# Kernel optimization log

Hardware: AMD Instinct MI355X
Metric: run time of the kernel (lower is better)

Reference implementation:

```python
import jax, jax.numpy as jnp
import numpy as np

NC = 1_000_000   # children
NP_ = 100_000    # parents
DIM = 64         # value/channel dim
H = 4            # heads
DQK = 8          # per-head query/key dim
DH = DQK * H     # 32
RPE = 9          # edge_attr feature dim
SCALE = DQK ** -0.5


def setup_inputs() -> dict:
    key = jax.random.key(0)
    ks = jax.random.split(key, 12)
    return {
        "x_child": jax.random.normal(ks[0], (NC, DIM), dtype=jnp.float32),
        "x_parent": jax.random.normal(ks[1], (NP_, DIM), dtype=jnp.float32),
        "index": jax.random.randint(ks[2], (NC,), 0, NP_, dtype=jnp.int64),
        "edge_attr": jax.random.normal(ks[3], (NC, RPE), dtype=jnp.float32),
        "wq": jax.random.normal(ks[4], (DIM, DH), dtype=jnp.float32) * 0.05,
        "bq": jax.random.normal(ks[5], (DH,), dtype=jnp.float32) * 0.05,
        "wkv": jax.random.normal(ks[6], (DIM, DH + DIM), dtype=jnp.float32) * 0.05,
        "bkv": jax.random.normal(ks[7], (DH + DIM,), dtype=jnp.float32) * 0.05,
        "wk_rpe": jax.random.normal(ks[8], (RPE, DH), dtype=jnp.float32) * 0.05,
        "bk_rpe": jax.random.normal(ks[9], (DH,), dtype=jnp.float32) * 0.05,
        "wq_rpe": jax.random.normal(ks[10], (RPE, DH), dtype=jnp.float32) * 0.05,
        "bq_rpe": jax.random.normal(ks[11], (DH,), dtype=jnp.float32) * 0.05,
    }


def reference(x_child, x_parent, index, edge_attr,
              wq, bq, wkv, bkv, wk_rpe, bk_rpe, wq_rpe, bq_rpe):
    Nc = x_child.shape[0]
    Np = x_parent.shape[0]
    # _get_query: Linear(Cp -> H*DQK) on parents, then gather per child edge
    q_parent = x_parent @ wq + bq                      # (Np, H*D)
    q = q_parent[index].reshape(Nc, H, DQK) * SCALE    # (Nc, H, D)
    # kv projection on children
    kv = x_child @ wkv + bkv                           # (Nc, H*D + DIM)
    k = kv[:, :DH].reshape(Nc, H, DQK)
    v = kv[:, DH:].reshape(Nc, H, DIM // H)
    # relative positional encodings added to k and q
    k = k + (edge_attr @ wk_rpe + bk_rpe).reshape(Nc, H, DQK)
    q = q + (edge_attr @ wq_rpe + bq_rpe).reshape(Nc, H, DQK)
    # per-edge compatibility, segment softmax grouped by parent index
    compat = jnp.einsum('nhd,nhd->nh', q, k)           # (Nc, H)
    m = jax.ops.segment_max(compat, index, num_segments=Np)   # (Np, H)
    e = jnp.exp(compat - m[index])
    s = jax.ops.segment_sum(e, index, num_segments=Np)        # (Np, H)
    attn = e / (s[index] + 1e-16)                      # (Nc, H)
    # weighted scatter-sum pooling
    xw = (v * attn[:, :, None]).reshape(Nc, DIM)       # (Nc, DIM)
    out = jax.ops.segment_sum(xw, index, num_segments=Np)     # (Np, DIM)
    return out
```

## Files before the change

kernel.cpp:

```cpp
#include <hip/hip_runtime.h>

#define NC    1000000
#define NPAR  100000
#define DIM   64
#define H     4
#define RPE   9
#define SCALE 0.35355339059327373f
#define CB    128
#define NBS   ((NPAR + 1023) / 1024)

typedef __attribute__((ext_vector_type(8))) short short8;
typedef __attribute__((ext_vector_type(4))) float f32x4;

__device__ inline unsigned short f2bf(float f) {
    unsigned int u = __float_as_uint(f);
    u += 0x7fff + ((u >> 16) & 1);
    return (unsigned short)(u >> 16);
}
__device__ inline unsigned int pack2bf(float a, float b) {
    return (unsigned int)f2bf(a) | ((unsigned int)f2bf(b) << 16);
}

__global__ __launch_bounds__(256) void qproj_kernel(const float* __restrict__ xp,
                             const float* __restrict__ wq,
                             const float* __restrict__ bq,
                             float* __restrict__ qp) {
    __shared__ float wqT[32 * 64];
    __shared__ float bqL[32];
    int tid = threadIdx.x;
    for (int i = tid; i < 2048; i += 256) { int o = i >> 6, j = i & 63; wqT[i] = wq[j * 32 + o]; }
    if (tid < 32) bqL[tid] = bq[tid];
    __syncthreads();
    int p = blockIdx.x * 256 + tid;
    if (p >= NPAR) return;
    float4 x4[16];
    const float4* xr = (const float4*)(xp + (size_t)p * 64);
#pragma unroll
    for (int i = 0; i < 16; ++i) x4[i] = xr[i];
    float* qpr = qp + (size_t)p * 32;
#pragma unroll 1
    for (int o = 0; o < 32; ++o) {
        float acc = bqL[o];
        const float4* w4 = (const float4*)(wqT + o * 64);
#pragma unroll
        for (int j = 0; j < 16; ++j) { float4 w = w4[j], xx = x4[j];
            acc += xx.x * w.x + xx.y * w.y + xx.z * w.z + xx.w * w.w; }
        qpr[o] = acc * SCALE;
    }
}

__global__ __launch_bounds__(256) void prepB_kernel(
    const float* __restrict__ wkv, const float* __restrict__ bkv,
    const float* __restrict__ wkr, const float* __restrict__ bkr,
    const float* __restrict__ wqr, const float* __restrict__ bqr,
    uint4* __restrict__ Bg) {
    int tid = threadIdx.x;
    for (int i = tid; i < 12 * 128; i += 256) {
        int kb = i >> 7, n = i & 127;
        float w[8];
#pragma unroll
        for (int jj = 0; jj < 8; ++jj) {
            int k = kb * 8 + jj;
            float val = 0.f;
            if (n < 32) {
                if (k < 64)       val = wkv[k * 96 + n];
                else if (k < 73)  val = wkr[(k - 64) * 32 + n];
                else if (k == 73) val = bkv[n] + bkr[n];
            } else if (n < 96) {
                int d = n - 32;
                if (k < 64)       val = wkv[k * 96 + 32 + d];
                else if (k == 73) val = bkv[32 + d];
            } else {
                int o = n - 96;
                if (k >= 64 && k < 73) val = wqr[(k - 64) * 32 + o];
                else if (k == 73)      val = bqr[o];
            }
            w[jj] = val;
        }
        uint4 v;
        v.x = pack2bf(w[0], w[1]); v.y = pack2bf(w[2], w[3]);
        v.z = pack2bf(w[4], w[5]); v.w = pack2bf(w[6], w[7]);
        Bg[kb * 128 + n] = v;
    }
}

__global__ __launch_bounds__(256) void hist_kernel(const int* __restrict__ index,
                            int* __restrict__ cnt) {
    int c = blockIdx.x * 256 + threadIdx.x;
    if (c >= NC) return;
    atomicAdd(&cnt[index[c]], 1);
}

__global__ __launch_bounds__(1024) void scanA_kernel(const int* __restrict__ cnt,
                                                     int* __restrict__ bsum) {
    __shared__ int red[16];
    int i = blockIdx.x * 1024 + threadIdx.x;
    int v = (i < NPAR) ? cnt[i] : 0;
#pragma unroll
    for (int off = 32; off; off >>= 1) v += __shfl_down(v, off, 64);
    if ((threadIdx.x & 63) == 0) red[threadIdx.x >> 6] = v;
    __syncthreads();
    if (threadIdx.x < 16) {
        int s = red[threadIdx.x];
#pragma unroll
        for (int off = 8; off; off >>= 1) s += __shfl_down(s, off, 16);
        if (threadIdx.x == 0) bsum[blockIdx.x] = s;
    }
}

__global__ __launch_bounds__(128) void scanB_kernel(int* __restrict__ bsum) {
    __shared__ int s[128];
    int t = threadIdx.x;
    int v = (t < NBS) ? bsum[t] : 0;
    s[t] = v;
    __syncthreads();
    for (int off = 1; off < 128; off <<= 1) {
        int x = s[t];
        int add = (t >= off) ? s[t - off] : 0;
        __syncthreads();
        s[t] = x + add;
        __syncthreads();
    }
    if (t < NBS) bsum[t] = s[t] - v;
}

__global__ __launch_bounds__(1024) void scanC_kernel(const int* __restrict__ cnt,
                                                     const int* __restrict__ bsum,
                                                     int* __restrict__ rowStart,
                                                     int* __restrict__ cursor) {
    __shared__ int s[1024];
    int t = threadIdx.x;
    int i = blockIdx.x * 1024 + t;
    int v = (i < NPAR) ? cnt[i] : 0;
    s[t] = v;
    __syncthreads();
    for (int off = 1; off < 1024; off <<= 1) {
        int x = s[t];
        int add = (t >= off) ? s[t - off] : 0;
        __syncthreads();
        s[t] = x + add;
        __syncthreads();
    }
    int excl = s[t] - v + bsum[blockIdx.x];
    if (i < NPAR) { rowStart[i] = excl; cursor[i] = excl; }
    if (i == NPAR - 1) rowStart[NPAR] = excl + v;
}

__global__ __launch_bounds__(256) void scatter_kernel(const int* __restrict__ index,
                               int* __restrict__ cursor,
                               int* __restrict__ order) {
    int c = blockIdx.x * 256 + threadIdx.x;
    if (c >= NC) return;
    order[atomicAdd(&cursor[index[c]], 1)] = c;
}

__global__ __launch_bounds__(256, 4) void fused_kernel(
    const float* __restrict__ xc, const float* __restrict__ ea_g,
    const int* __restrict__ index, const int* __restrict__ order,
    const int* __restrict__ rowStart,
    const uint4* __restrict__ Bg,
    const float* __restrict__ qp,
    float* __restrict__ outw, float* __restrict__ sW)
{
    __shared__ __align__(16) char R1[34816];
    __shared__ float e_lds[CB * 4];
    __shared__ int par_s[CB];
    __shared__ int wcnt[4];
    __shared__ int segStart[130];

    uint4* A4 = (uint4*)R1;
    float* kqT = (float*)R1;
    float* wvS = (float*)R1;

    const int tid  = threadIdx.x;
    const int lane = tid & 63, wave = tid >> 6;
    const int col  = lane & 15, quad = lane >> 4;
    const int G    = blockIdx.x * CB;
    const int validCB = min(NC - G, CB);

    {
        const int half = tid >> 7;
        const int c = tid & 127;
        const bool valid = c < validCB;
        int ch = 0, p = 0x7fffffff;
        if (valid) { ch = order[G + c]; p = index[ch]; }
        if (half == 0) {
            par_s[c] = p;
            float4 x4[10];
            if (valid) {
                const float4* xr = (const float4*)(xc + (size_t)ch * 64);
#pragma unroll
                for (int i = 0; i < 10; ++i) x4[i] = xr[i];
            } else {
#pragma unroll
                for (int i = 0; i < 10; ++i) x4[i] = make_float4(0.f, 0.f, 0.f, 0.f);
            }
#pragma unroll
            for (int kb = 0; kb < 5; ++kb) {
                uint4 v;
                v.x = pack2bf(x4[kb * 2].x, x4[kb * 2].y);
                v.y = pack2bf(x4[kb * 2].z, x4[kb * 2].w);
                v.z = pack2bf(x4[kb * 2 + 1].x, x4[kb * 2 + 1].y);
                v.w = pack2bf(x4[kb * 2 + 1].z, x4[kb * 2 + 1].w);
                A4[kb * 128 + c] = v;
            }
        } else {
            float4 x4[6];
            float ear[9];
            if (valid) {
                const float4* xr = (const float4*)(xc + (size_t)ch * 64);
#pragma unroll
                for (int i = 0; i < 6; ++i) x4[i] = xr[10 + i];
                const float* er = ea_g + (size_t)ch * 9;
#pragma unroll
                for (int r = 0; r < 9; ++r) ear[r] = er[r];
            } else {
#pragma unroll
                for (int i = 0; i < 6; ++i) x4[i] = make_float4(0.f, 0.f, 0.f, 0.f);
#pragma unroll
                for (int r = 0; r < 9; ++r) ear[r] = 0.f;
            }
#pragma unroll
            for (int kb = 0; kb < 3; ++kb) {
                uint4 v;
                v.x = pack2bf(x4[kb * 2].x, x4[kb * 2].y);
                v.y = pack2bf(x4[kb * 2].z, x4[kb * 2].w);
                v.z = pack2bf(x4[kb * 2 + 1].x, x4[kb * 2 + 1].y);
                v.w = pack2bf(x4[kb * 2 + 1].z, x4[kb * 2 + 1].w);
                A4[(5 + kb) * 128 + c] = v;
            }
            {
                uint4 v;
                v.x = pack2bf(ear[0], ear[1]); v.y = pack2bf(ear[2], ear[3]);
                v.z = pack2bf(ear[4], ear[5]); v.w = pack2bf(ear[6], ear[7]);
                A4[8 * 128 + c] = v;
            }
            {
                uint4 v;
                v.x = pack2bf(ear[8], valid ? 1.f : 0.f);
                v.y = 0u; v.z = 0u; v.w = 0u;
                A4[9 * 128 + c] = v;
            }
        }
    }
    __syncthreads();

    f32x4 acc[2][8];
#pragma unroll
    for (int mt = 0; mt < 2; ++mt)
#pragma unroll
        for (int nt = 0; nt < 8; ++nt) acc[mt][nt] = (f32x4){0.f, 0.f, 0.f, 0.f};
    const int wbase = wave * 32;
    const short8* As = (const short8*)A4;
    const short8* Bs = (const short8*)Bg;
    const short8 zero8 = {0, 0, 0, 0, 0, 0, 0, 0};
#pragma unroll 1
    for (int ks = 0; ks < 3; ++ks) {
        const int kb = ks * 4 + quad;
        short8 af0 = zero8, af1 = zero8;
        if (kb < 10) {
            af0 = As[kb * 128 + wbase + col];
            af1 = As[kb * 128 + wbase + 16 + col];
        }
        short8 bf[8];
#pragma unroll
        for (int nt = 0; nt < 6; ++nt) bf[nt] = Bs[kb * 128 + nt * 16 + col];
#pragma unroll
        for (int nt = 0; nt < 6; ++nt) {
            acc[0][nt] = __builtin_amdgcn_mfma_f32_16x16x32_bf16(af0, bf[nt], acc[0][nt], 0, 0, 0);
            acc[1][nt] = __builtin_amdgcn_mfma_f32_16x16x32_bf16(af1, bf[nt], acc[1][nt], 0, 0, 0);
        }
        if (ks == 2) {
#pragma unroll
            for (int nt = 6; nt < 8; ++nt) {
                short8 b2 = Bs[kb * 128 + nt * 16 + col];
                acc[0][nt] = __builtin_amdgcn_mfma_f32_16x16x32_bf16(af0, b2, acc[0][nt], 0, 0, 0);
                acc[1][nt] = __builtin_amdgcn_mfma_f32_16x16x32_bf16(af1, b2, acc[1][nt], 0, 0, 0);
            }
        }
    }
    __syncthreads();

#pragma unroll
    for (int mt = 0; mt < 2; ++mt) {
        int cb = wbase + mt * 16 + quad * 4;
#pragma unroll
        for (int nt = 0; nt < 2; ++nt) {
            int nl = nt * 16 + col;
            *(f32x4*)(kqT + nl * 132 + cb) = acc[mt][nt];
        }
#pragma unroll
        for (int nt = 6; nt < 8; ++nt) {
            int nl = 32 + (nt - 6) * 16 + col;
            *(f32x4*)(kqT + nl * 132 + cb) = acc[mt][nt];
        }
    }
    __syncthreads();

    {
        const int c = tid;
        bool valid = c < validCB;
        int p = 0x7fffffff;
        if (valid) p = par_s[c];
        float e0 = 0.f, e1 = 0.f, e2 = 0.f, e3 = 0.f;
        if (valid) {
            const float* qpr = qp + (size_t)p * 32;
            float qv[32];
#pragma unroll
            for (int i = 0; i < 8; ++i) *(float4*)(qv + 4 * i) = ((const float4*)qpr)[i];
            float comp[4] = {0.f, 0.f, 0.f, 0.f};
#pragma unroll
            for (int o = 0; o < 32; ++o) {
                float kk = kqT[o * 132 + c];
                float qq = qv[o] + kqT[(32 + o) * 132 + c];
                comp[o >> 3] += qq * kk;
            }
            e0 = __expf(comp[0]); e1 = __expf(comp[1]);
            e2 = __expf(comp[2]); e3 = __expf(comp[3]);
        }
        if (c < CB) *(float4*)(e_lds + c * 4) = make_float4(e0, e1, e2, e3);

        bool ishead = valid && (c == 0 || par_s[c - 1] != p);
        unsigned long long mask = __ballot(ishead);
        if (lane == 0) wcnt[wave] = __popcll(mask);
        __syncthreads();
        int base = 0;
#pragma unroll
        for (int w = 0; w < 4; ++w) if (w < wave) base += wcnt[w];
        if (ishead) segStart[base + __popcll(mask & ((1ull << lane) - 1))] = c;
        if (tid == 0) {
            int ns = wcnt[0] + wcnt[1] + wcnt[2] + wcnt[3];
            segStart[ns] = validCB;
            segStart[129] = ns;
        }
    }

#pragma unroll
    for (int mt = 0; mt < 2; ++mt) {
        int cb = wbase + mt * 16 + quad * 4;
#pragma unroll
        for (int nt = 2; nt < 6; ++nt) {
            int d = (nt - 2) * 16 + col;
            int h = nt - 2;
#pragma unroll
            for (int r = 0; r < 4; ++r) {
                float e = e_lds[(cb + r) * 4 + h];
                wvS[(cb + r) * 68 + d] = acc[mt][nt][r] * e;
            }
        }
    }
    __syncthreads();

    {
        int nseg = segStart[129];
        for (int s = wave; s < nseg; s += 4) {
            int a = segStart[s], b = segStart[s + 1];
            int p = par_s[a];
            int d = lane, h = lane >> 4;
            float vs = 0.f, es = 0.f;
            for (int c2 = a; c2 < b; ++c2) {
                vs += wvS[c2 * 68 + d];
                es += e_lds[c2 * 4 + h];
            }
            bool full = (rowStart[p] == G + a) && (rowStart[p + 1] == G + b);
            if (full) {
                outw[(size_t)p * 64 + d] = vs;
                if ((d & 15) == 0) sW[(size_t)p * 4 + h] = es;
            } else {
                atomicAdd(&outw[(size_t)p * 64 + d], vs);
                if ((d & 15) == 0) atomicAdd(&sW[(size_t)p * 4 + h], es);
            }
        }
    }
}

__global__ __launch_bounds__(256) void norm_kernel(const float* __restrict__ sW,
                                                   float* __restrict__ out) {
    int t = blockIdx.x * 256 + threadIdx.x;
    if (t >= NPAR * 64) return;
    out[t] = out[t] / (sW[(t >> 6) * 4 + ((t >> 4) & 3)] + 1e-16f);
}

extern "C" void kernel_launch(void* const* d_in, const int* in_sizes, int n_in,
                              void* d_out, int out_size, void* d_ws, size_t ws_size,
                              hipStream_t stream) {
    const float* xc   = (const float*)d_in[0];
    const float* xp   = (const float*)d_in[1];
    const int*   idx  = (const int*)d_in[2];
    const float* ea   = (const float*)d_in[3];
    const float* wq   = (const float*)d_in[4];
    const float* bq   = (const float*)d_in[5];
    const float* wkv  = (const float*)d_in[6];
    const float* bkv  = (const float*)d_in[7];
    const float* wkr  = (const float*)d_in[8];
    const float* bkr  = (const float*)d_in[9];
    const float* wqr  = (const float*)d_in[10];
    const float* bqr  = (const float*)d_in[11];
    float* out = (float*)d_out;

    char* base = (char*)d_ws;
    size_t off = 0;
    auto alloc = [&](size_t bytes) {
        void* r = base + off;
        off += (bytes + 255) & ~(size_t)255;
        return r;
    };
    float* qp       = (float*)alloc((size_t)NPAR * 32 * sizeof(float));
    int*   cnt      = (int*)  alloc((size_t)NPAR * sizeof(int));
    int*   rowStart = (int*)  alloc(((size_t)NPAR + 1) * sizeof(int));
    int*   cursor   = (int*)  alloc((size_t)NPAR * sizeof(int));
    int*   order    = (int*)  alloc((size_t)NC * sizeof(int));
    float* sW       = (float*)alloc((size_t)NPAR * 4 * sizeof(float));
    int*   bsum     = (int*)  alloc((size_t)NBS * sizeof(int));
    uint4* Bg       = (uint4*)alloc((size_t)12 * 128 * sizeof(uint4));
    (void)ws_size;

    hipMemsetAsync(cnt, 0, (size_t)NPAR * sizeof(int), stream);
    hipMemsetAsync(sW,  0, (size_t)NPAR * 4 * sizeof(float), stream);
    hipMemsetAsync(out, 0, (size_t)NPAR * 64 * sizeof(float), stream);

    qproj_kernel  <<<(NPAR + 255) / 256, 256, 0, stream>>>(xp, wq, bq, qp);
    prepB_kernel  <<<1,                  256, 0, stream>>>(wkv, bkv, wkr, bkr, wqr, bqr, Bg);
    hist_kernel   <<<(NC + 255) / 256,   256, 0, stream>>>(idx, cnt);
    scanA_kernel  <<<NBS,               1024, 0, stream>>>(cnt, bsum);
    scanB_kernel  <<<1,                  128, 0, stream>>>(bsum);
    scanC_kernel  <<<NBS,               1024, 0, stream>>>(cnt, bsum, rowStart, cursor);
    scatter_kernel<<<(NC + 255) / 256,   256, 0, stream>>>(idx, cursor, order);
    fused_kernel  <<<(NC + CB - 1) / CB, 256, 0, stream>>>(xc, ea, idx, order, rowStart,
                                                           Bg, qp, out, sW);
    norm_kernel   <<<(NPAR * 64 + 255) / 256, 256, 0, stream>>>(sW, out);
}
```

Baseline: 660.1 us.

## Store child and parent together in sort order and compute scores from MFMA registers

The scatter kernel now writes (child, parent) pairs, so the fused kernel no longer does a dependent random gather of index[child] after reading the order array. The q·k compatibility is now computed straight from the MFMA accumulator registers, using per-lane q loads and cross-lane shuffle reductions. This removes the LDS transpose store, a barrier, and the column-wise LDS reads. The cost is twice the bytes for the order array and more scattered small global loads of qp per lane.

```diff
diff --git a/kernel.cpp b/kernel.cpp
--- a/kernel.cpp
+++ b/kernel.cpp
@@ -148,15 +148,17 @@
 
 __global__ __launch_bounds__(256) void scatter_kernel(const int* __restrict__ index,
                                int* __restrict__ cursor,
-                               int* __restrict__ order) {
+                               int2* __restrict__ ordCP) {
     int c = blockIdx.x * 256 + threadIdx.x;
     if (c >= NC) return;
-    order[atomicAdd(&cursor[index[c]], 1)] = c;
+    int p = index[c];
+    int pos = atomicAdd(&cursor[p], 1);
+    ordCP[pos] = make_int2(c, p);
 }
 
 __global__ __launch_bounds__(256, 4) void fused_kernel(
     const float* __restrict__ xc, const float* __restrict__ ea_g,
-    const int* __restrict__ index, const int* __restrict__ order,
+    const int2* __restrict__ ordCP,
     const int* __restrict__ rowStart,
     const uint4* __restrict__ Bg,
     const float* __restrict__ qp,
@@ -169,7 +171,6 @@
     __shared__ int segStart[130];
 
     uint4* A4 = (uint4*)R1;
-    float* kqT = (float*)R1;
     float* wvS = (float*)R1;
 
     const int tid  = threadIdx.x;
@@ -183,7 +184,7 @@
         const int c = tid & 127;
         const bool valid = c < validCB;
         int ch = 0, p = 0x7fffffff;
-        if (valid) { ch = order[G + c]; p = index[ch]; }
+        if (valid) { int2 cp = ordCP[G + c]; ch = cp.x; p = cp.y; }
         if (half == 0) {
             par_s[c] = p;
             float4 x4[10];
@@ -281,46 +282,45 @@
     }
     __syncthreads();
 
-#pragma unroll
-    for (int mt = 0; mt < 2; ++mt) {
-        int cb = wbase + mt * 16 + quad * 4;
-#pragma unroll
-        for (int nt = 0; nt < 2; ++nt) {
-            int nl = nt * 16 + col;
-            *(f32x4*)(kqT + nl * 132 + cb) = acc[mt][nt];
-        }
-#pragma unroll
-        for (int nt = 6; nt < 8; ++nt) {
-            int nl = 32 + (nt - 6) * 16 + col;
-            *(f32x4*)(kqT + nl * 132 + cb) = acc[mt][nt];
-        }
-    }
-    __syncthreads();
-
     {
+        float comp[2][4][2];
+#pragma unroll
+        for (int mt = 0; mt < 2; ++mt) {
+#pragma unroll
+            for (int r = 0; r < 4; ++r) {
+                int cc = wbase + mt * 16 + quad * 4 + r;
+                int p = par_s[cc];
+                if (p >= NPAR) p = 0;
+                const float* qpr = qp + (size_t)p * 32;
+#pragma unroll
+                for (int nt = 0; nt < 2; ++nt) {
+                    float q = qpr[nt * 16 + col] + acc[mt][nt + 6][r];
+                    comp[mt][r][nt] = acc[mt][nt][r] * q;
+                }
+            }
+        }
+#pragma unroll
+        for (int m = 1; m < 8; m <<= 1) {
+#pragma unroll
+            for (int mt = 0; mt < 2; ++mt)
+#pragma unroll
+                for (int r = 0; r < 4; ++r)
+#pragma unroll
+                    for (int nt = 0; nt < 2; ++nt)
+                        comp[mt][r][nt] += __shfl_xor(comp[mt][r][nt], m, 64);
+        }
+        {
+            int idx = col & 7;
+            int mtS = idx >> 2, rS = idx & 3;
+            int cS = wbase + mtS * 16 + quad * 4 + rS;
+            int hb = col >> 3;
+            bool v0 = cS < validCB;
+            e_lds[cS * 4 + hb]     = v0 ? __expf(comp[mtS][rS][0]) : 0.f;
+            e_lds[cS * 4 + 2 + hb] = v0 ? __expf(comp[mtS][rS][1]) : 0.f;
+        }
         const int c = tid;
-        bool valid = c < validCB;
-        int p = 0x7fffffff;
-        if (valid) p = par_s[c];
-        float e0 = 0.f, e1 = 0.f, e2 = 0.f, e3 = 0.f;
-        if (valid) {
-            const float* qpr = qp + (size_t)p * 32;
-            float qv[32];
-#pragma unroll
-            for (int i = 0; i < 8; ++i) *(float4*)(qv + 4 * i) = ((const float4*)qpr)[i];
-            float comp[4] = {0.f, 0.f, 0.f, 0.f};
-#pragma unroll
-            for (int o = 0; o < 32; ++o) {
-                float kk = kqT[o * 132 + c];
-                float qq = qv[o] + kqT[(32 + o) * 132 + c];
-                comp[o >> 3] += qq * kk;
-            }
-            e0 = __expf(comp[0]); e1 = __expf(comp[1]);
-            e2 = __expf(comp[2]); e3 = __expf(comp[3]);
-        }
-        if (c < CB) *(float4*)(e_lds + c * 4) = make_float4(e0, e1, e2, e3);
-
-        bool ishead = valid && (c == 0 || par_s[c - 1] != p);
+        bool valid = (c < validCB);
+        bool ishead = valid && (c == 0 || par_s[c - 1] != par_s[c]);
         unsigned long long mask = __ballot(ishead);
         if (lane == 0) wcnt[wave] = __popcll(mask);
         __syncthreads();
@@ -409,7 +409,7 @@
     int*   cnt      = (int*)  alloc((size_t)NPAR * sizeof(int));
     int*   rowStart = (int*)  alloc(((size_t)NPAR + 1) * sizeof(int));
     int*   cursor   = (int*)  alloc((size_t)NPAR * sizeof(int));
-    int*   order    = (int*)  alloc((size_t)NC * sizeof(int));
+    int2*  ordCP    = (int2*) alloc((size_t)NC * sizeof(int2));
     float* sW       = (float*)alloc((size_t)NPAR * 4 * sizeof(float));
     int*   bsum     = (int*)  alloc((size_t)NBS * sizeof(int));
     uint4* Bg       = (uint4*)alloc((size_t)12 * 128 * sizeof(uint4));
@@ -425,8 +425,8 @@
     scanA_kernel  <<<NBS,               1024, 0, stream>>>(cnt, bsum);
     scanB_kernel  <<<1,                  128, 0, stream>>>(bsum);
     scanC_kernel  <<<NBS,               1024, 0, stream>>>(cnt, bsum, rowStart, cursor);
-    scatter_kernel<<<(NC + 255) / 256,   256, 0, stream>>>(idx, cursor, order);
-    fused_kernel  <<<(NC + CB - 1) / CB, 256, 0, stream>>>(xc, ea, idx, order, rowStart,
+    scatter_kernel<<<(NC + 255) / 256,   256, 0, stream>>>(idx, cursor, ordCP);
+    fused_kernel  <<<(NC + CB - 1) / CB, 256, 0, stream>>>(xc, ea, ordCP, rowStart,
                                                            Bg, qp, out, sW);
     norm_kernel   <<<(NPAR * 64 + 255) / 256, 256, 0, stream>>>(sW, out);
 }
```

Measured after the change: 677.9 us. +2.7%, slower.
